# Kernel tuning notes

Hardware: AMD Instinct MI355X
Metric: run time of the kernel (lower is better)

## Reference

```python
import jax, jax.numpy as jnp
import numpy as np

B, IN, OUT = 4096, 1024, 1024
HALF_PI = np.pi / 2.0
TWO_PI = 2.0 * np.pi
# cyclic control-point index table per quadrant (from the torch module)
CPI = jnp.array([[3, 0, 1, 2], [0, 1, 2, 3], [1, 2, 3, 0], [2, 3, 0, 1]], dtype=jnp.int32)
# Catmull-Rom cubic spline basis (4 control points, [t^3,t^2,t,1] monomials)
BASIS = np.array([[-0.5, 1.5, -1.5, 0.5],
                  [1.0, -2.5, 2.0, -0.5],
                  [-0.5, 0.0, 0.5, 0.0],
                  [0.0, 1.0, 0.0, 0.0]], dtype=np.float32)


def setup_inputs() -> dict:
    key = jax.random.key(0)
    k_x, k_p, k_w, k_b = jax.random.split(key, 4)
    x = jax.random.normal(k_x, (B, IN), dtype=jnp.float32)
    phase = jax.random.uniform(k_p, (B,), dtype=jnp.float32) * TWO_PI
    # kaiming_uniform_(a=sqrt(5)) on each (OUT, IN) slice -> bound = 1/sqrt(fan_in)
    bound = 1.0 / np.sqrt(IN)
    weights = jax.random.uniform(k_w, (4, OUT, IN), dtype=jnp.float32, minval=-bound, maxval=bound)
    biases = jax.random.uniform(k_b, (4, OUT), dtype=jnp.float32, minval=-bound, maxval=bound)
    basis = jnp.asarray(BASIS)
    return {"input": x, "phase": phase, "weights": weights, "biases": biases, "basis": basis}


def reference(input, phase, weights, biases, basis):
    # quadrant index q in {0,1,2,3}; same selection as the nested torch.where chain
    q = jnp.clip(jnp.floor(phase / HALF_PI).astype(jnp.int32), 0, 3)          # (B,)
    t = phase / HALF_PI - q.astype(phase.dtype)                                # (B,), in [0,1)
    tt = jnp.stack([t ** 3, t ** 2, t, jnp.ones_like(t)], axis=-1)             # (B,4)
    coeffs = tt @ basis                                                        # (B,4) spline coeffs
    idx = CPI[q]                                                               # (B,4) control-point ids
    # Instead of materializing per-sample (B,OUT,IN) weights, contract input against
    # all 4 control-point matrices (same math: w_b = sum_k c_k W_{idx_k}).
    z = jnp.einsum('bi,coi->bco', input, weights)                              # (B,4,OUT)
    zg = jnp.take_along_axis(z, idx[:, :, None], axis=1)                       # (B,4,OUT)
    bg = biases[idx]                                                           # (B,4,OUT)
    return jnp.einsum('bk,bko->bo', coeffs, zg + bg)                           # (B,OUT)
```

## Files before the change

### kernel.cpp

```cpp
#include <hip/hip_runtime.h>
#include <stdint.h>

#define BATCH   4096
#define IN_DIM  1024
#define OUT_DIM 1024

typedef __bf16 bf16x8 __attribute__((ext_vector_type(8)));
typedef float  f32x4  __attribute__((ext_vector_type(4)));

__device__ __forceinline__ uint16_t f2bf(float f) {
    union { float f; uint32_t u; } v; v.f = f;
    uint32_t u = v.u;
    uint32_t r = (u + 0x7FFFu + ((u >> 16) & 1u)) >> 16;
    return (uint16_t)r;
}

__device__ __forceinline__ float bf2f(uint16_t h) {
    union { uint32_t u; float f; } v; v.u = ((uint32_t)h) << 16;
    return v.f;
}

__global__ __launch_bounds__(256) void prep(
    const float* __restrict__ x, const float* __restrict__ phase,
    const float* __restrict__ basis, const float* __restrict__ W,
    uint16_t* __restrict__ xb, uint16_t* __restrict__ Wb,
    float* __restrict__ alphaWS)
{
    const int bid = blockIdx.x;
    const int tid = threadIdx.x;

    if (bid < BATCH) {
        const int b = bid;
        const float HALF_PI = 1.5707963267948966f;
        float s  = phase[b] / HALF_PI;
        int   q  = (int)floorf(s);
        q = q < 0 ? 0 : (q > 3 ? 3 : q);
        float t  = s - (float)q;
        float t2 = t * t, t3 = t2 * t;

        float coef[4];
#pragma unroll
        for (int j = 0; j < 4; ++j)
            coef[j] = t3 * basis[j] + t2 * basis[4 + j] + t * basis[8 + j] + basis[12 + j];

        if (tid < 4) alphaWS[b * 4 + tid] = coef[(tid - q + 1) & 3];

        float4 xv = ((const float4*)(x + (size_t)b * IN_DIM))[tid];
        ushort4 o;
        o.x = f2bf(xv.x); o.y = f2bf(xv.y); o.z = f2bf(xv.z); o.w = f2bf(xv.w);
        ((ushort4*)(xb + (size_t)b * IN_DIM))[tid] = o;
    } else {
        const int j = bid - BATCH;
        float4 wv = ((const float4*)W)[j * 256 + tid];
        ushort4 o;
        o.x = f2bf(wv.x); o.y = f2bf(wv.y); o.z = f2bf(wv.z); o.w = f2bf(wv.w);
        ((ushort4*)Wb)[j * 256 + tid] = o;
    }
}

#define PS 66

__global__ __launch_bounds__(256, 3) void gemm_fused(
    const uint16_t* __restrict__ xb, const uint16_t* __restrict__ Wb,
    const float* __restrict__ alphaWS, const float* __restrict__ biases,
    float* __restrict__ out)
{
    __shared__ uint16_t lds[64 * 64 + 4 * 64 * 64];
    uint16_t* As = lds;
    uint16_t* Bs = lds + 4096;
    uint16_t* Ps = lds;

    const int tid  = threadIdx.x;
    const int lane = tid & 63;
    const int wid  = tid >> 6;
    const int tileM = blockIdx.x * 64;
    const int tileN = blockIdx.y * 64;

    f32x4 acc[4][4];
#pragma unroll
    for (int mi = 0; mi < 4; ++mi)
#pragma unroll
        for (int ni = 0; ni < 4; ++ni)
            acc[mi][ni] = (f32x4){0.f, 0.f, 0.f, 0.f};

    const int srow = lane >> 3;
    const int gchunk = ((lane & 7) ^ srow) * 8;

    const uint16_t* Ag = xb + (size_t)tileM * 1024;
    const uint16_t* Bg = Wb + ((size_t)wid << 20) + (size_t)tileN * 1024;

    const int quad = lane >> 4;
    const int l7   = lane & 7;

    for (int kt = 0; kt < 16; ++kt) {
        const int k0 = kt * 64;
#pragma unroll
        for (int j = 0; j < 2; ++j) {
            const int s = wid * 2 + j;
            const uint16_t* ga = Ag + (size_t)(s * 8 + srow) * 1024 + k0 + gchunk;
            __builtin_amdgcn_global_load_lds(
                (const __attribute__((address_space(1))) void*)ga,
                (__attribute__((address_space(3))) void*)(As + s * 512), 16, 0, 0);
        }
#pragma unroll
        for (int j = 0; j < 8; ++j) {
            const uint16_t* gb = Bg + (size_t)(j * 8 + srow) * 1024 + k0 + gchunk;
            __builtin_amdgcn_global_load_lds(
                (const __attribute__((address_space(1))) void*)gb,
                (__attribute__((address_space(3))) void*)(Bs + wid * 4096 + j * 512), 16, 0, 0);
        }
        __syncthreads();

#pragma unroll
        for (int ks = 0; ks < 2; ++ks) {
            const int ch = (ks * 4 + quad) ^ l7;
            bf16x8 af[4], bfr[4];
#pragma unroll
            for (int mi = 0; mi < 4; ++mi) {
                const int row = mi * 16 + (lane & 15);
                af[mi] = *(const bf16x8*)(As + row * 64 + ch * 8);
            }
#pragma unroll
            for (int ni = 0; ni < 4; ++ni) {
                const int row = ni * 16 + (lane & 15);
                bfr[ni] = *(const bf16x8*)(Bs + wid * 4096 + row * 64 + ch * 8);
            }
#pragma unroll
            for (int mi = 0; mi < 4; ++mi)
#pragma unroll
                for (int ni = 0; ni < 4; ++ni)
                    acc[mi][ni] = __builtin_amdgcn_mfma_f32_16x16x32_bf16(
                        af[mi], bfr[ni], acc[mi][ni], 0, 0, 0);
        }
        __syncthreads();
    }

    float av[4][4];
#pragma unroll
    for (int mi = 0; mi < 4; ++mi)
#pragma unroll
        for (int r = 0; r < 4; ++r)
            av[mi][r] = alphaWS[(size_t)(tileM + mi * 16 + quad * 4 + r) * 4 + wid];

#pragma unroll
    for (int mi = 0; mi < 4; ++mi) {
#pragma unroll
        for (int r = 0; r < 4; ++r) {
            const int row = mi * 16 + quad * 4 + r;
#pragma unroll
            for (int ni = 0; ni < 4; ++ni)
                Ps[wid * (64 * PS) + row * PS + ni * 16 + (lane & 15)] =
                    f2bf(av[mi][r] * acc[mi][ni][r]);
        }
    }
    __syncthreads();

    {
        const int rr = tid >> 2;
        const int cg = tid & 3;
        const int colb = cg * 16;
        const float4 al = *(const float4*)(alphaWS + (size_t)(tileM + rr) * 4);
        const float a[4] = {al.x, al.y, al.z, al.w};

        float res[16];
#pragma unroll
        for (int j = 0; j < 16; ++j) res[j] = 0.f;

#pragma unroll
        for (int cc = 0; cc < 4; ++cc) {
#pragma unroll
            for (int jj = 0; jj < 4; ++jj) {
                float4 bv = *(const float4*)(biases + (size_t)cc * OUT_DIM + tileN + colb + jj * 4);
                res[jj * 4 + 0] += a[cc] * bv.x;
                res[jj * 4 + 1] += a[cc] * bv.y;
                res[jj * 4 + 2] += a[cc] * bv.z;
                res[jj * 4 + 3] += a[cc] * bv.w;
            }
            const uint16_t* p = Ps + cc * (64 * PS) + rr * PS + colb;
#pragma unroll
            for (int jj = 0; jj < 8; ++jj) {
                uint32_t pv = *(const uint32_t*)(p + jj * 2);
                res[jj * 2 + 0] += bf2f((uint16_t)(pv & 0xFFFFu));
                res[jj * 2 + 1] += bf2f((uint16_t)(pv >> 16));
            }
        }

        float* orow = out + (size_t)(tileM + rr) * OUT_DIM + tileN + colb;
#pragma unroll
        for (int jj = 0; jj < 4; ++jj) {
            float4 o = {res[jj * 4 + 0], res[jj * 4 + 1], res[jj * 4 + 2], res[jj * 4 + 3]};
            *(float4*)(orow + jj * 4) = o;
        }
    }
}

extern "C" void kernel_launch(void* const* d_in, const int* in_sizes, int n_in,
                              void* d_out, int out_size, void* d_ws, size_t ws_size,
                              hipStream_t stream)
{
    const float* x       = (const float*)d_in[0];
    const float* phase   = (const float*)d_in[1];
    const float* weights = (const float*)d_in[2];
    const float* biases  = (const float*)d_in[3];
    const float* basis   = (const float*)d_in[4];
    float* out = (float*)d_out;

    uint16_t* xb = (uint16_t*)d_ws;
    uint16_t* Wb = xb + (size_t)BATCH * IN_DIM;
    float* alphaWS = (float*)(Wb + (size_t)4 * OUT_DIM * IN_DIM);

    prep<<<2 * BATCH, 256, 0, stream>>>(x, phase, basis, weights, xb, Wb, alphaWS);

    dim3 grid(BATCH / 64, OUT_DIM / 64);
    gemm_fused<<<grid, 256, 0, stream>>>(xb, Wb, alphaWS, biases, out);
}
```

Before: 130.0 us.

## Double M tile to 128 with 8 waves sharing weight tiles

The GEMM block grows from 64 to 128 batch rows and from 4 to 8 waves. The two wave halves share the same four control-point weight tiles loaded into LDS, which halves the weight traffic per output. The epilogue now runs in two passes that reuse the partial-product LDS region, with extra barriers between them. The cost is a larger LDS footprint and more synchronisation in the epilogue, and occupancy may change at 512 threads per block.

```diff
diff --git a/kernel.cpp b/kernel.cpp
--- a/kernel.cpp
+++ b/kernel.cpp
@@ -60,20 +60,22 @@
 
 #define PS 66
 
-__global__ __launch_bounds__(256, 3) void gemm_fused(
+__global__ __launch_bounds__(512, 4) void gemm_fused(
     const uint16_t* __restrict__ xb, const uint16_t* __restrict__ Wb,
     const float* __restrict__ alphaWS, const float* __restrict__ biases,
     float* __restrict__ out)
 {
-    __shared__ uint16_t lds[64 * 64 + 4 * 64 * 64];
+    __shared__ uint16_t lds[128 * 64 + 4 * 64 * 64];
     uint16_t* As = lds;
-    uint16_t* Bs = lds + 4096;
+    uint16_t* Bs = lds + 8192;
     uint16_t* Ps = lds;
 
     const int tid  = threadIdx.x;
     const int lane = tid & 63;
     const int wid  = tid >> 6;
-    const int tileM = blockIdx.x * 64;
+    const int cw   = wid & 3;
+    const int mh   = wid >> 2;
+    const int tileM = blockIdx.x * 128;
     const int tileN = blockIdx.y * 64;
 
     f32x4 acc[4][4];
@@ -87,7 +89,6 @@
     const int gchunk = ((lane & 7) ^ srow) * 8;
 
     const uint16_t* Ag = xb + (size_t)tileM * 1024;
-    const uint16_t* Bg = Wb + ((size_t)wid << 20) + (size_t)tileN * 1024;
 
     const int quad = lane >> 4;
     const int l7   = lane & 7;
@@ -103,11 +104,15 @@
                 (__attribute__((address_space(3))) void*)(As + s * 512), 16, 0, 0);
         }
 #pragma unroll
-        for (int j = 0; j < 8; ++j) {
-            const uint16_t* gb = Bg + (size_t)(j * 8 + srow) * 1024 + k0 + gchunk;
+        for (int j = 0; j < 4; ++j) {
+            const int g  = wid * 4 + j;
+            const int cb = g >> 3;
+            const int sr = g & 7;
+            const uint16_t* gb = Wb + ((size_t)cb << 20)
+                               + (size_t)(tileN + sr * 8 + srow) * 1024 + k0 + gchunk;
             __builtin_amdgcn_global_load_lds(
                 (const __attribute__((address_space(1))) void*)gb,
-                (__attribute__((address_space(3))) void*)(Bs + wid * 4096 + j * 512), 16, 0, 0);
+                (__attribute__((address_space(3))) void*)(Bs + cb * 4096 + sr * 512), 16, 0, 0);
         }
         __syncthreads();
 
@@ -117,13 +122,13 @@
             bf16x8 af[4], bfr[4];
 #pragma unroll
             for (int mi = 0; mi < 4; ++mi) {
-                const int row = mi * 16 + (lane & 15);
+                const int row = mh * 64 + mi * 16 + (lane & 15);
                 af[mi] = *(const bf16x8*)(As + row * 64 + ch * 8);
             }
 #pragma unroll
             for (int ni = 0; ni < 4; ++ni) {
                 const int row = ni * 16 + (lane & 15);
-                bfr[ni] = *(const bf16x8*)(Bs + wid * 4096 + row * 64 + ch * 8);
+                bfr[ni] = *(const bf16x8*)(Bs + cw * 4096 + row * 64 + ch * 8);
             }
 #pragma unroll
             for (int mi = 0; mi < 4; ++mi)
@@ -140,57 +145,59 @@
     for (int mi = 0; mi < 4; ++mi)
 #pragma unroll
         for (int r = 0; r < 4; ++r)
-            av[mi][r] = alphaWS[(size_t)(tileM + mi * 16 + quad * 4 + r) * 4 + wid];
-
-#pragma unroll
-    for (int mi = 0; mi < 4; ++mi) {
-#pragma unroll
-        for (int r = 0; r < 4; ++r) {
-            const int row = mi * 16 + quad * 4 + r;
-#pragma unroll
-            for (int ni = 0; ni < 4; ++ni)
-                Ps[wid * (64 * PS) + row * PS + ni * 16 + (lane & 15)] =
-                    f2bf(av[mi][r] * acc[mi][ni][r]);
-        }
-    }
-    __syncthreads();
-
-    {
-        const int rr = tid >> 2;
-        const int cg = tid & 3;
-        const int colb = cg * 16;
-        const float4 al = *(const float4*)(alphaWS + (size_t)(tileM + rr) * 4);
+            av[mi][r] = alphaWS[(size_t)(tileM + mh * 64 + mi * 16 + quad * 4 + r) * 4 + cw];
+
+    const int rr   = tid >> 3;
+    const int colb = (tid & 7) * 8;
+
+#pragma unroll
+    for (int p = 0; p < 2; ++p) {
+        __syncthreads();
+        if (mh == p) {
+#pragma unroll
+            for (int mi = 0; mi < 4; ++mi) {
+#pragma unroll
+                for (int r = 0; r < 4; ++r) {
+                    const int row = mi * 16 + quad * 4 + r;
+#pragma unroll
+                    for (int ni = 0; ni < 4; ++ni)
+                        Ps[cw * (64 * PS) + row * PS + ni * 16 + (lane & 15)] =
+                            f2bf(av[mi][r] * acc[mi][ni][r]);
+                }
+            }
+        }
+        __syncthreads();
+
+        const int m = tileM + p * 64 + rr;
+        const float4 al = *(const float4*)(alphaWS + (size_t)m * 4);
         const float a[4] = {al.x, al.y, al.z, al.w};
 
-        float res[16];
-#pragma unroll
-        for (int j = 0; j < 16; ++j) res[j] = 0.f;
+        float res[8];
+#pragma unroll
+        for (int j = 0; j < 8; ++j) res[j] = 0.f;
 
 #pragma unroll
         for (int cc = 0; cc < 4; ++cc) {
+            float4 b0 = *(const float4*)(biases + (size_t)cc * OUT_DIM + tileN + colb);
+            float4 b1 = *(const float4*)(biases + (size_t)cc * OUT_DIM + tileN + colb + 4);
+            res[0] += a[cc] * b0.x; res[1] += a[cc] * b0.y;
+            res[2] += a[cc] * b0.z; res[3] += a[cc] * b0.w;
+            res[4] += a[cc] * b1.x; res[5] += a[cc] * b1.y;
+            res[6] += a[cc] * b1.z; res[7] += a[cc] * b1.w;
+            const uint16_t* pp = Ps + cc * (64 * PS) + rr * PS + colb;
 #pragma unroll
             for (int jj = 0; jj < 4; ++jj) {
-                float4 bv = *(const float4*)(biases + (size_t)cc * OUT_DIM + tileN + colb + jj * 4);
-                res[jj * 4 + 0] += a[cc] * bv.x;
-                res[jj * 4 + 1] += a[cc] * bv.y;
-                res[jj * 4 + 2] += a[cc] * bv.z;
-                res[jj * 4 + 3] += a[cc] * bv.w;
-            }
-            const uint16_t* p = Ps + cc * (64 * PS) + rr * PS + colb;
-#pragma unroll
-            for (int jj = 0; jj < 8; ++jj) {
-                uint32_t pv = *(const uint32_t*)(p + jj * 2);
+                uint32_t pv = *(const uint32_t*)(pp + jj * 2);
                 res[jj * 2 + 0] += bf2f((uint16_t)(pv & 0xFFFFu));
                 res[jj * 2 + 1] += bf2f((uint16_t)(pv >> 16));
             }
         }
 
-        float* orow = out + (size_t)(tileM + rr) * OUT_DIM + tileN + colb;
-#pragma unroll
-        for (int jj = 0; jj < 4; ++jj) {
-            float4 o = {res[jj * 4 + 0], res[jj * 4 + 1], res[jj * 4 + 2], res[jj * 4 + 3]};
-            *(float4*)(orow + jj * 4) = o;
-        }
+        float* orow = out + (size_t)m * OUT_DIM + tileN + colb;
+        float4 o0 = {res[0], res[1], res[2], res[3]};
+        float4 o1 = {res[4], res[5], res[6], res[7]};
+        *(float4*)(orow)     = o0;
+        *(float4*)(orow + 4) = o1;
     }
 }
 
@@ -211,6 +218,6 @@
 
     prep<<<2 * BATCH, 256, 0, stream>>>(x, phase, basis, weights, xb, Wb, alphaWS);
 
-    dim3 grid(BATCH / 64, OUT_DIM / 64);
-    gemm_fused<<<grid, 256, 0, stream>>>(xb, Wb, alphaWS, biases, out);
-}
+    dim3 grid(BATCH / 128, OUT_DIM / 64);
+    gemm_fused<<<grid, 512, 0, stream>>>(xb, Wb, alphaWS, biases, out);
+}
```

Result: slower. 171.0 us (+31.6%).
